# Kernel optimization log

Hardware: AMD Instinct MI355X
Metric: run time of the kernel (lower is better)

Reference implementation:

```python
import jax, jax.numpy as jnp
import numpy as np

B, N, QDIM, KVDIM, DIM, H = 2, 4096, 256, 256, 256, 8


def setup_inputs() -> dict:
    key = jax.random.key(0)
    ks = jax.random.split(key, 8)
    s = 0.02
    return {
        "x": jax.random.normal(ks[0], (B, N, QDIM), jnp.float32),
        "y": jax.random.normal(ks[1], (B, N, KVDIM), jnp.float32),
        "Wq": jax.random.normal(ks[2], (DIM, QDIM), jnp.float32) * s,
        "bq": jnp.zeros((DIM,), jnp.float32),
        "Wk": jax.random.normal(ks[3], (DIM, KVDIM), jnp.float32) * s,
        "bk": jnp.zeros((DIM,), jnp.float32),
        "Wv": jax.random.normal(ks[4], (DIM, KVDIM), jnp.float32) * s,
        "bv": jnp.zeros((DIM,), jnp.float32),
        "Wo": jax.random.normal(ks[5], (DIM, DIM), jnp.float32) * s,
        "bo": jnp.zeros((DIM,), jnp.float32),
    }


def reference(x, y, Wq, bq, Wk, bk, Wv, bv, Wo, bo):
    b, n, _ = x.shape
    h = H
    scale = KVDIM ** (-0.5)  # note: full kv_dim, as in the source
    q = x @ Wq.T + bq  # (b, n, dim)
    k = y @ Wk.T + bk
    v = y @ Wv.T + bv
    def split(t):
        return t.reshape(b, -1, h, DIM // h).transpose(0, 2, 1, 3)  # b h n d
    q, k, v = split(q), split(k), split(v)
    dots = jnp.einsum('bhid,bhjd->bhij', q, k) * scale
    attn = jax.nn.softmax(dots, axis=-1)
    out = jnp.einsum('bhij,bhjd->bhid', attn, v)
    out = out.transpose(0, 2, 1, 3).reshape(b, n, DIM)  # b n (h d)
    out = out @ Wo.T + bo
    return out
```

## Files before the change

kernel.cpp:

```cpp
#include <hip/hip_runtime.h>

#define BATCH 2
#define SEQ   4096
#define DIM   256
#define NHEAD 8
#define HDIM  32
#define ROWS  (BATCH * SEQ)

typedef __attribute__((ext_vector_type(8))) short short8;
typedef __attribute__((ext_vector_type(8))) unsigned short ushort8;
typedef __attribute__((ext_vector_type(4))) unsigned short ushortx4;
typedef __attribute__((ext_vector_type(4))) float floatx4;

static __device__ __forceinline__ unsigned short f2bf(float f) {
    union { float f; unsigned u; } v; v.f = f;
    unsigned r = v.u + 0x7fffu + ((v.u >> 16) & 1u);
    return (unsigned short)(r >> 16);
}

static __device__ __forceinline__ void g2l16(const void* g, void* l) {
    __builtin_amdgcn_global_load_lds(
        (const __attribute__((address_space(1))) unsigned int*)g,
        (__attribute__((address_space(3))) unsigned int*)l, 16, 0, 0);
}

__global__ __launch_bounds__(256) void convw_kernel(
    const float* __restrict__ W0, const float* __restrict__ W1,
    const float* __restrict__ W2, const float* __restrict__ W3,
    unsigned short* __restrict__ o0, unsigned short* __restrict__ o1,
    unsigned short* __restrict__ o2, unsigned short* __restrict__ o3) {
    const float* s; unsigned short* d;
    switch (blockIdx.y) {
        case 0:  s = W0; d = o0; break;
        case 1:  s = W1; d = o1; break;
        case 2:  s = W2; d = o2; break;
        default: s = W3; d = o3; break;
    }
    long off = ((long)blockIdx.x * 256 + threadIdx.x) * 4;
    float4 v = *(const float4*)(s + off);
    ushortx4 o;
    o.x = f2bf(v.x); o.y = f2bf(v.y); o.z = f2bf(v.z); o.w = f2bf(v.w);
    *(ushortx4*)(d + off) = o;
}

__global__ __launch_bounds__(256, 2) void qkv_kernel(
    const float* __restrict__ x, const float* __restrict__ y,
    const unsigned short* __restrict__ Wq, const unsigned short* __restrict__ Wk,
    const unsigned short* __restrict__ Wv,
    const float* __restrict__ bq, const float* __restrict__ bk, const float* __restrict__ bv,
    unsigned short* __restrict__ qo, unsigned short* __restrict__ ko,
    unsigned short* __restrict__ vto) {
    __shared__ unsigned short Abuf[8][64][32];
    const int tid = threadIdx.x, lane = tid & 63, wave = tid >> 6;
    const int ql = lane & 15, quad = lane >> 4;
    const int mat = blockIdx.y;
    const int m0 = blockIdx.x * 64;
    const float* A = (mat == 0) ? x : y;
    const unsigned short* W = (mat == 0) ? Wq : (mat == 1) ? Wk : Wv;
    const float* bias = (mat == 0) ? bq : (mat == 1) ? bk : bv;

    {
        const int row = tid >> 2, c8 = (tid & 3) * 8;
        const float* src = A + (long)(m0 + row) * DIM + c8;
#pragma unroll
        for (int kb = 0; kb < 8; kb++) {
            float4 v0 = *(const float4*)(src + kb * 32);
            float4 v1 = *(const float4*)(src + kb * 32 + 4);
            ushort8 o;
            o[0] = f2bf(v0.x); o[1] = f2bf(v0.y); o[2] = f2bf(v0.z); o[3] = f2bf(v0.w);
            o[4] = f2bf(v1.x); o[5] = f2bf(v1.y); o[6] = f2bf(v1.z); o[7] = f2bf(v1.w);
            *(ushort8*)(&Abuf[kb][row][c8]) = o;
        }
    }
    __syncthreads();
    const int n0 = wave * 64;
    floatx4 acc[4][4] = {};
    if (mat < 2) {
        for (int kb = 0; kb < 8; kb++) {
            short8 wf[4], af[4];
#pragma unroll
            for (int u = 0; u < 4; u++)
                wf[u] = *(const short8*)(W + (long)(n0 + u*16 + ql) * DIM + kb*32 + quad*8);
#pragma unroll
            for (int t = 0; t < 4; t++)
                af[t] = *(const short8*)(&Abuf[kb][t*16 + ql][quad*8]);
#pragma unroll
            for (int t = 0; t < 4; t++)
#pragma unroll
                for (int u = 0; u < 4; u++)
                    acc[t][u] = __builtin_amdgcn_mfma_f32_16x16x32_bf16(wf[u], af[t], acc[t][u], 0, 0, 0);
        }
        const float scale = (mat == 0) ? 0.09016844005556021f : 1.0f;
        unsigned short* out = (mat == 0) ? qo : ko;
#pragma unroll
        for (int t = 0; t < 4; t++) {
            int m = m0 + t*16 + ql;
#pragma unroll
            for (int u = 0; u < 4; u++) {
                int n = n0 + u*16 + quad*4;
                float4 b4 = *(const float4*)(bias + n);
                ushortx4 o;
                o.x = f2bf((acc[t][u][0] + b4.x) * scale);
                o.y = f2bf((acc[t][u][1] + b4.y) * scale);
                o.z = f2bf((acc[t][u][2] + b4.z) * scale);
                o.w = f2bf((acc[t][u][3] + b4.w) * scale);
                *(ushortx4*)(out + (long)m * DIM + n) = o;
            }
        }
    } else {
        for (int kb = 0; kb < 8; kb++) {
            short8 wf[4], af[4];
#pragma unroll
            for (int u = 0; u < 4; u++)
                wf[u] = *(const short8*)(W + (long)(n0 + u*16 + ql) * DIM + kb*32 + quad*8);
#pragma unroll
            for (int t = 0; t < 4; t++)
                af[t] = *(const short8*)(&Abuf[kb][t*16 + ql][quad*8]);
#pragma unroll
            for (int t = 0; t < 4; t++)
#pragma unroll
                for (int u = 0; u < 4; u++)
                    acc[t][u] = __builtin_amdgcn_mfma_f32_16x16x32_bf16(af[t], wf[u], acc[t][u], 0, 0, 0);
        }
#pragma unroll
        for (int t = 0; t < 4; t++) {
            int mb = m0 + t*16 + quad*4;
            int bi = mb >> 12, i0 = mb & (SEQ - 1);
#pragma unroll
            for (int u = 0; u < 4; u++) {
                int n = n0 + u*16 + ql;
                float b = bias[n];
                ushortx4 o;
                o.x = f2bf(acc[t][u][0] + b);
                o.y = f2bf(acc[t][u][1] + b);
                o.z = f2bf(acc[t][u][2] + b);
                o.w = f2bf(acc[t][u][3] + b);
                *(ushortx4*)(vto + ((long)(bi * DIM + n)) * SEQ + i0) = o;
            }
        }
    }
}

__global__ __launch_bounds__(256, 2) void attn_kernel(
    const unsigned short* __restrict__ qb, const unsigned short* __restrict__ kbuf,
    const unsigned short* __restrict__ vT, unsigned short* __restrict__ ao) {
    __shared__ unsigned short K0[128 * 32], K1[128 * 32];
    __shared__ unsigned short V0[32 * 128], V1[32 * 128];
    __shared__ unsigned short P[4][32][72];
    const int tid = threadIdx.x, lane = tid & 63, wave = tid >> 6;
    const int ql = lane & 15, quad = lane >> 4;
    const int bh = blockIdx.y, b = bh >> 3, h = bh & 7;
    const int q0 = blockIdx.x * 128 + wave * 32;

    const unsigned short* qrow = qb   + (long)b * SEQ * DIM + h * HDIM;
    const unsigned short* krow = kbuf + (long)b * SEQ * DIM + h * HDIM;
    const unsigned short* vrow = vT   + (long)(b * DIM + h * HDIM) * SEQ;

    short8 qf[2];
#pragma unroll
    for (int t = 0; t < 2; t++)
        qf[t] = *(const short8*)(qrow + (long)(q0 + t*16 + ql) * DIM + quad*8);

    const int kc0 = wave * 2, kc1 = wave * 2 + 1;
    const unsigned short* kg0 = krow + (long)(kc0*16 + (lane >> 2)) * DIM + (lane & 3) * 8;
    const unsigned short* kg1 = krow + (long)(kc1*16 + (lane >> 2)) * DIM + (lane & 3) * 8;
    const unsigned short* vg0 = vrow + (long)(kc0*4 + (lane >> 4)) * SEQ + (lane & 15) * 8;
    const unsigned short* vg1 = vrow + (long)(kc1*4 + (lane >> 4)) * SEQ + (lane & 15) * 8;

    floatx4 acc[2][2] = {};
    float lp[2] = {0.f, 0.f};

    auto stage = [&](unsigned short* Kd, unsigned short* Vd, int kv0) {
        g2l16(kg0 + (long)kv0 * DIM, Kd + kc0 * 512);
        g2l16(kg1 + (long)kv0 * DIM, Kd + kc1 * 512);
        g2l16(vg0 + kv0, Vd + kc0 * 512);
        g2l16(vg1 + kv0, Vd + kc1 * 512);
    };
    auto compute = [&](const unsigned short* Ks, const unsigned short* Vs) {
#pragma unroll
        for (int half = 0; half < 2; ++half) {
#pragma unroll
            for (int mt = 0; mt < 4; ++mt) {
                short8 kf = *(const short8*)(Ks + (half*64 + mt*16 + ql) * 32 + quad*8);
#pragma unroll
                for (int t = 0; t < 2; t++) {
                    floatx4 z = {};
                    floatx4 s = __builtin_amdgcn_mfma_f32_16x16x32_bf16(kf, qf[t], z, 0, 0, 0);
                    float p0 = __builtin_amdgcn_exp2f(s[0]);
                    float p1 = __builtin_amdgcn_exp2f(s[1]);
                    float p2 = __builtin_amdgcn_exp2f(s[2]);
                    float p3 = __builtin_amdgcn_exp2f(s[3]);
                    lp[t] += (p0 + p1) + (p2 + p3);
                    ushortx4 o;
                    o.x = f2bf(p0); o.y = f2bf(p1); o.z = f2bf(p2); o.w = f2bf(p3);
                    *(ushortx4*)(&P[wave][t*16 + ql][mt*16 + quad*4]) = o;
                }
            }
#pragma unroll
            for (int ks = 0; ks < 2; ++ks) {
                short8 pf[2];
#pragma unroll
                for (int t = 0; t < 2; t++)
                    pf[t] = *(const short8*)(&P[wave][t*16 + ql][ks*32 + quad*8]);
#pragma unroll
                for (int dt = 0; dt < 2; ++dt) {
                    short8 vf = *(const short8*)(Vs + (dt*16 + ql) * 128 + half*64 + ks*32 + quad*8);
#pragma unroll
                    for (int t = 0; t < 2; t++)
                        acc[dt][t] = __builtin_amdgcn_mfma_f32_16x16x32_bf16(vf, pf[t], acc[dt][t], 0, 0, 0);
                }
            }
        }
    };

    stage(K0, V0, 0);
    __syncthreads();
    for (int it = 0; it < SEQ / 128; it += 2) {
        if (it + 1 < SEQ / 128) stage(K1, V1, (it + 1) * 128);
        compute(K0, V0);
        __syncthreads();
        if (it + 2 < SEQ / 128) stage(K0, V0, (it + 2) * 128);
        compute(K1, V1);
        __syncthreads();
    }

    float inv[2];
#pragma unroll
    for (int t = 0; t < 2; t++) {
        float l = lp[t];
        l += __shfl_xor(l, 16, 64);
        l += __shfl_xor(l, 32, 64);
        inv[t] = 1.0f / l;
    }
#pragma unroll
    for (int dt = 0; dt < 2; dt++)
#pragma unroll
        for (int t = 0; t < 2; t++) {
            ushortx4 o;
            o.x = f2bf(acc[dt][t][0] * inv[t]);
            o.y = f2bf(acc[dt][t][1] * inv[t]);
            o.z = f2bf(acc[dt][t][2] * inv[t]);
            o.w = f2bf(acc[dt][t][3] * inv[t]);
            *(ushortx4*)(ao + (long)(b*SEQ + q0 + t*16 + ql) * DIM + h*HDIM + dt*16 + quad*4) = o;
        }
}

__global__ __launch_bounds__(256, 2) void oproj_kernel(
    const unsigned short* __restrict__ A, const unsigned short* __restrict__ W,
    const float* __restrict__ bias, float* __restrict__ out) {
    __shared__ unsigned short Abuf[8][64][32];
    const int tid = threadIdx.x, lane = tid & 63, wave = tid >> 6;
    const int ql = lane & 15, quad = lane >> 4;
    const int m0 = blockIdx.x * 64;
#pragma unroll
    for (int j = 0; j < 8; j++) {
        int c = wave * 8 + j;
        int kb = c >> 2, r0 = (c & 3) * 16;
        const unsigned short* g = A + (long)(m0 + r0 + (lane >> 2)) * DIM + kb*32 + (lane & 3) * 8;
        g2l16(g, &Abuf[kb][r0][0]);
    }
    __syncthreads();
    const int n0 = wave * 64;
    floatx4 acc[4][4] = {};
    for (int kb = 0; kb < 8; kb++) {
        short8 wf[4], af[4];
#pragma unroll
        for (int u = 0; u < 4; u++)
            wf[u] = *(const short8*)(W + (long)(n0 + u*16 + ql) * DIM + kb*32 + quad*8);
#pragma unroll
        for (int t = 0; t < 4; t++)
            af[t] = *(const short8*)(&Abuf[kb][t*16 + ql][quad*8]);
#pragma unroll
        for (int t = 0; t < 4; t++)
#pragma unroll
            for (int u = 0; u < 4; u++)
                acc[t][u] = __builtin_amdgcn_mfma_f32_16x16x32_bf16(wf[u], af[t], acc[t][u], 0, 0, 0);
    }
#pragma unroll
    for (int t = 0; t < 4; t++) {
        int m = m0 + t*16 + ql;
#pragma unroll
        for (int u = 0; u < 4; u++) {
            int n = n0 + u*16 + quad*4;
            float4 b4 = *(const float4*)(bias + n);
            float4 o;
            o.x = acc[t][u][0] + b4.x;
            o.y = acc[t][u][1] + b4.y;
            o.z = acc[t][u][2] + b4.z;
            o.w = acc[t][u][3] + b4.w;
            *(float4*)(out + (long)m * DIM + n) = o;
        }
    }
}

extern "C" void kernel_launch(void* const* d_in, const int* in_sizes, int n_in,
                              void* d_out, int out_size, void* d_ws, size_t ws_size,
                              hipStream_t stream) {
    const float* x  = (const float*)d_in[0];
    const float* y  = (const float*)d_in[1];
    const float* Wq = (const float*)d_in[2];
    const float* bq = (const float*)d_in[3];
    const float* Wk = (const float*)d_in[4];
    const float* bk = (const float*)d_in[5];
    const float* Wv = (const float*)d_in[6];
    const float* bv = (const float*)d_in[7];
    const float* Wo = (const float*)d_in[8];
    const float* bo = (const float*)d_in[9];
    float* out = (float*)d_out;

    const long NX = (long)ROWS * DIM;
    const long NW = (long)DIM * DIM;
    unsigned short* Wqb  = (unsigned short*)d_ws;
    unsigned short* Wkb  = Wqb + NW;
    unsigned short* Wvb  = Wkb + NW;
    unsigned short* Wob  = Wvb + NW;
    unsigned short* qbf  = Wob + NW;
    unsigned short* kbf  = qbf + NX;
    unsigned short* vTb  = kbf + NX;
    unsigned short* attn = vTb + NX;

    convw_kernel<<<dim3(NW / 1024, 4), dim3(256), 0, stream>>>(
        Wq, Wk, Wv, Wo, Wqb, Wkb, Wvb, Wob);

    qkv_kernel<<<dim3(ROWS / 64, 3), dim3(256), 0, stream>>>(
        x, y, Wqb, Wkb, Wvb, bq, bk, bv, qbf, kbf, vTb);

    attn_kernel<<<dim3(SEQ / 128, BATCH * NHEAD), dim3(256), 0, stream>>>(
        qbf, kbf, vTb, attn);

    oproj_kernel<<<dim3(ROWS / 64), dim3(256), 0, stream>>>(
        attn, Wob, bo, out);
}
```

Before: 189.8 us.

## Fuse weight conversion into GEMMs, swizzle LDS, compute softmax row sums via MFMA

```diff
diff --git a/kernel.cpp b/kernel.cpp
--- a/kernel.cpp
+++ b/kernel.cpp
@@ -11,12 +11,19 @@
 typedef __attribute__((ext_vector_type(8))) unsigned short ushort8;
 typedef __attribute__((ext_vector_type(4))) unsigned short ushortx4;
 typedef __attribute__((ext_vector_type(4))) float floatx4;
+typedef __attribute__((ext_vector_type(2))) unsigned int uintx2;
 
 static __device__ __forceinline__ unsigned short f2bf(float f) {
     union { float f; unsigned u; } v; v.f = f;
     unsigned r = v.u + 0x7fffu + ((v.u >> 16) & 1u);
     return (unsigned short)(r >> 16);
 }
+static __device__ __forceinline__ unsigned fbits(float f) {
+    union { float f; unsigned u; } v; v.f = f; return v.u;
+}
+static __device__ __forceinline__ unsigned pack2(float a, float b) {
+    return __builtin_amdgcn_perm(fbits(b), fbits(a), 0x07060302u);
+}
 
 static __device__ __forceinline__ void g2l16(const void* g, void* l) {
     __builtin_amdgcn_global_load_lds(
@@ -24,29 +31,10 @@
         (__attribute__((address_space(3))) unsigned int*)l, 16, 0, 0);
 }
 
-__global__ __launch_bounds__(256) void convw_kernel(
-    const float* __restrict__ W0, const float* __restrict__ W1,
-    const float* __restrict__ W2, const float* __restrict__ W3,
-    unsigned short* __restrict__ o0, unsigned short* __restrict__ o1,
-    unsigned short* __restrict__ o2, unsigned short* __restrict__ o3) {
-    const float* s; unsigned short* d;
-    switch (blockIdx.y) {
-        case 0:  s = W0; d = o0; break;
-        case 1:  s = W1; d = o1; break;
-        case 2:  s = W2; d = o2; break;
-        default: s = W3; d = o3; break;
-    }
-    long off = ((long)blockIdx.x * 256 + threadIdx.x) * 4;
-    float4 v = *(const float4*)(s + off);
-    ushortx4 o;
-    o.x = f2bf(v.x); o.y = f2bf(v.y); o.z = f2bf(v.z); o.w = f2bf(v.w);
-    *(ushortx4*)(d + off) = o;
-}
-
 __global__ __launch_bounds__(256, 2) void qkv_kernel(
     const float* __restrict__ x, const float* __restrict__ y,
-    const unsigned short* __restrict__ Wq, const unsigned short* __restrict__ Wk,
-    const unsigned short* __restrict__ Wv,
+    const float* __restrict__ Wq, const float* __restrict__ Wk,
+    const float* __restrict__ Wv,
     const float* __restrict__ bq, const float* __restrict__ bk, const float* __restrict__ bv,
     unsigned short* __restrict__ qo, unsigned short* __restrict__ ko,
     unsigned short* __restrict__ vto) {
@@ -56,11 +44,12 @@
     const int mat = blockIdx.y;
     const int m0 = blockIdx.x * 64;
     const float* A = (mat == 0) ? x : y;
-    const unsigned short* W = (mat == 0) ? Wq : (mat == 1) ? Wk : Wv;
+    const float* W = (mat == 0) ? Wq : (mat == 1) ? Wk : Wv;
     const float* bias = (mat == 0) ? bq : (mat == 1) ? bk : bv;
 
     {
         const int row = tid >> 2, c8 = (tid & 3) * 8;
+        const int swz = ((tid & 3) ^ ((row >> 1) & 3)) * 8;
         const float* src = A + (long)(m0 + row) * DIM + c8;
 #pragma unroll
         for (int kb = 0; kb < 8; kb++) {
@@ -69,27 +58,43 @@
             ushort8 o;
             o[0] = f2bf(v0.x); o[1] = f2bf(v0.y); o[2] = f2bf(v0.z); o[3] = f2bf(v0.w);
             o[4] = f2bf(v1.x); o[5] = f2bf(v1.y); o[6] = f2bf(v1.z); o[7] = f2bf(v1.w);
-            *(ushort8*)(&Abuf[kb][row][c8]) = o;
+            *(ushort8*)(&Abuf[kb][row][swz]) = o;
         }
     }
     __syncthreads();
     const int n0 = wave * 64;
+    const int akey = (quad ^ ((ql >> 1) & 3)) * 8;
     floatx4 acc[4][4] = {};
-    if (mat < 2) {
-        for (int kb = 0; kb < 8; kb++) {
-            short8 wf[4], af[4];
-#pragma unroll
-            for (int u = 0; u < 4; u++)
-                wf[u] = *(const short8*)(W + (long)(n0 + u*16 + ql) * DIM + kb*32 + quad*8);
-#pragma unroll
-            for (int t = 0; t < 4; t++)
-                af[t] = *(const short8*)(&Abuf[kb][t*16 + ql][quad*8]);
+    for (int kb = 0; kb < 8; kb++) {
+        short8 wf[4], af[4];
+#pragma unroll
+        for (int u = 0; u < 4; u++) {
+            const float* wr = W + (long)(n0 + u*16 + ql) * DIM + kb*32 + quad*8;
+            float4 a = *(const float4*)wr;
+            float4 c = *(const float4*)(wr + 4);
+            short8 o;
+            o[0] = (short)f2bf(a.x); o[1] = (short)f2bf(a.y); o[2] = (short)f2bf(a.z); o[3] = (short)f2bf(a.w);
+            o[4] = (short)f2bf(c.x); o[5] = (short)f2bf(c.y); o[6] = (short)f2bf(c.z); o[7] = (short)f2bf(c.w);
+            wf[u] = o;
+        }
+#pragma unroll
+        for (int t = 0; t < 4; t++)
+            af[t] = *(const short8*)(&Abuf[kb][t*16 + ql][akey]);
+        if (mat < 2) {
 #pragma unroll
             for (int t = 0; t < 4; t++)
 #pragma unroll
                 for (int u = 0; u < 4; u++)
                     acc[t][u] = __builtin_amdgcn_mfma_f32_16x16x32_bf16(wf[u], af[t], acc[t][u], 0, 0, 0);
-        }
+        } else {
+#pragma unroll
+            for (int t = 0; t < 4; t++)
+#pragma unroll
+                for (int u = 0; u < 4; u++)
+                    acc[t][u] = __builtin_amdgcn_mfma_f32_16x16x32_bf16(af[t], wf[u], acc[t][u], 0, 0, 0);
+        }
+    }
+    if (mat < 2) {
         const float scale = (mat == 0) ? 0.09016844005556021f : 1.0f;
         unsigned short* out = (mat == 0) ? qo : ko;
 #pragma unroll
@@ -108,20 +113,6 @@
             }
         }
     } else {
-        for (int kb = 0; kb < 8; kb++) {
-            short8 wf[4], af[4];
-#pragma unroll
-            for (int u = 0; u < 4; u++)
-                wf[u] = *(const short8*)(W + (long)(n0 + u*16 + ql) * DIM + kb*32 + quad*8);
-#pragma unroll
-            for (int t = 0; t < 4; t++)
-                af[t] = *(const short8*)(&Abuf[kb][t*16 + ql][quad*8]);
-#pragma unroll
-            for (int t = 0; t < 4; t++)
-#pragma unroll
-                for (int u = 0; u < 4; u++)
-                    acc[t][u] = __builtin_amdgcn_mfma_f32_16x16x32_bf16(af[t], wf[u], acc[t][u], 0, 0, 0);
-        }
 #pragma unroll
         for (int t = 0; t < 4; t++) {
             int mb = m0 + t*16 + quad*4;
@@ -161,14 +152,25 @@
     for (int t = 0; t < 2; t++)
         qf[t] = *(const short8*)(qrow + (long)(q0 + t*16 + ql) * DIM + quad*8);
 
+    short8 ones;
+#pragma unroll
+    for (int i = 0; i < 8; i++) ones[i] = (short)0x3F80;
+
     const int kc0 = wave * 2, kc1 = wave * 2 + 1;
-    const unsigned short* kg0 = krow + (long)(kc0*16 + (lane >> 2)) * DIM + (lane & 3) * 8;
-    const unsigned short* kg1 = krow + (long)(kc1*16 + (lane >> 2)) * DIM + (lane & 3) * 8;
-    const unsigned short* vg0 = vrow + (long)(kc0*4 + (lane >> 4)) * SEQ + (lane & 15) * 8;
-    const unsigned short* vg1 = vrow + (long)(kc1*4 + (lane >> 4)) * SEQ + (lane & 15) * 8;
+    const int klr = lane >> 2, kswz = ((lane & 3) ^ ((lane >> 3) & 3)) * 8;
+    const unsigned short* kg0 = krow + (long)(kc0*16 + klr) * DIM + kswz;
+    const unsigned short* kg1 = krow + (long)(kc1*16 + klr) * DIM + kswz;
+    const int vlr = lane >> 4, vcl = lane & 15;
+    const int vsw0 = (vcl ^ ((kc0*4 + vlr) & 7)) * 8;
+    const int vsw1 = (vcl ^ ((kc1*4 + vlr) & 7)) * 8;
+    const unsigned short* vg0 = vrow + (long)(kc0*4 + vlr) * SEQ + vsw0;
+    const unsigned short* vg1 = vrow + (long)(kc1*4 + vlr) * SEQ + vsw1;
+
+    const int kro = (quad ^ ((ql >> 1) & 3)) * 8;
+    const int vmask = ql & 7;
 
     floatx4 acc[2][2] = {};
-    float lp[2] = {0.f, 0.f};
+    floatx4 accL[2] = {};
 
     auto stage = [&](unsigned short* Kd, unsigned short* Vd, int kv0) {
         g2l16(kg0 + (long)kv0 * DIM, Kd + kc0 * 512);
@@ -181,7 +183,7 @@
         for (int half = 0; half < 2; ++half) {
 #pragma unroll
             for (int mt = 0; mt < 4; ++mt) {
-                short8 kf = *(const short8*)(Ks + (half*64 + mt*16 + ql) * 32 + quad*8);
+                short8 kf = *(const short8*)(Ks + (half*64 + mt*16 + ql) * 32 + kro);
 #pragma unroll
                 for (int t = 0; t < 2; t++) {
                     floatx4 z = {};
@@ -190,10 +192,10 @@
                     float p1 = __builtin_amdgcn_exp2f(s[1]);
                     float p2 = __builtin_amdgcn_exp2f(s[2]);
                     float p3 = __builtin_amdgcn_exp2f(s[3]);
-                    lp[t] += (p0 + p1) + (p2 + p3);
-                    ushortx4 o;
-                    o.x = f2bf(p0); o.y = f2bf(p1); o.z = f2bf(p2); o.w = f2bf(p3);
-                    *(ushortx4*)(&P[wave][t*16 + ql][mt*16 + quad*4]) = o;
+                    uintx2 w;
+                    w.x = pack2(p0, p1);
+                    w.y = pack2(p2, p3);
+                    *(uintx2*)(&P[wave][t*16 + ql][mt*16 + quad*4]) = w;
                 }
             }
 #pragma unroll
@@ -203,8 +205,12 @@
                 for (int t = 0; t < 2; t++)
                     pf[t] = *(const short8*)(&P[wave][t*16 + ql][ks*32 + quad*8]);
 #pragma unroll
+                for (int t = 0; t < 2; t++)
+                    accL[t] = __builtin_amdgcn_mfma_f32_16x16x32_bf16(ones, pf[t], accL[t], 0, 0, 0);
+#pragma unroll
                 for (int dt = 0; dt < 2; ++dt) {
-                    short8 vf = *(const short8*)(Vs + (dt*16 + ql) * 128 + half*64 + ks*32 + quad*8);
+                    int vco = ((8*half + 4*ks + quad) ^ vmask) * 8;
+                    short8 vf = *(const short8*)(Vs + (dt*16 + ql) * 128 + vco);
 #pragma unroll
                     for (int t = 0; t < 2; t++)
                         acc[dt][t] = __builtin_amdgcn_mfma_f32_16x16x32_bf16(vf, pf[t], acc[dt][t], 0, 0, 0);
@@ -226,12 +232,7 @@
 
     float inv[2];
 #pragma unroll
-    for (int t = 0; t < 2; t++) {
-        float l = lp[t];
-        l += __shfl_xor(l, 16, 64);
-        l += __shfl_xor(l, 32, 64);
-        inv[t] = 1.0f / l;
-    }
+    for (int t = 0; t < 2; t++) inv[t] = 1.0f / accL[t][0];
 #pragma unroll
     for (int dt = 0; dt < 2; dt++)
 #pragma unroll
@@ -246,38 +247,47 @@
 }
 
 __global__ __launch_bounds__(256, 2) void oproj_kernel(
-    const unsigned short* __restrict__ A, const unsigned short* __restrict__ W,
+    const unsigned short* __restrict__ A, const float* __restrict__ W,
     const float* __restrict__ bias, float* __restrict__ out) {
-    __shared__ unsigned short Abuf[8][64][32];
+    __shared__ unsigned short Abuf[8][32][32];
     const int tid = threadIdx.x, lane = tid & 63, wave = tid >> 6;
     const int ql = lane & 15, quad = lane >> 4;
-    const int m0 = blockIdx.x * 64;
-#pragma unroll
-    for (int j = 0; j < 8; j++) {
-        int c = wave * 8 + j;
-        int kb = c >> 2, r0 = (c & 3) * 16;
-        const unsigned short* g = A + (long)(m0 + r0 + (lane >> 2)) * DIM + kb*32 + (lane & 3) * 8;
-        g2l16(g, &Abuf[kb][r0][0]);
+    const int m0 = blockIdx.x * 32;
+    const int swz = ((lane & 3) ^ ((lane >> 3) & 3)) * 8;
+#pragma unroll
+    for (int j = 0; j < 4; j++) {
+        int c = wave * 4 + j;
+        int kb = c >> 1, hf = (c & 1) * 16;
+        const unsigned short* g = A + (long)(m0 + hf + (lane >> 2)) * DIM + kb*32 + swz;
+        g2l16(g, &Abuf[kb][hf][0]);
     }
     __syncthreads();
     const int n0 = wave * 64;
-    floatx4 acc[4][4] = {};
+    const int akey = (quad ^ ((ql >> 1) & 3)) * 8;
+    floatx4 acc[2][4] = {};
     for (int kb = 0; kb < 8; kb++) {
-        short8 wf[4], af[4];
-#pragma unroll
-        for (int u = 0; u < 4; u++)
-            wf[u] = *(const short8*)(W + (long)(n0 + u*16 + ql) * DIM + kb*32 + quad*8);
-#pragma unroll
-        for (int t = 0; t < 4; t++)
-            af[t] = *(const short8*)(&Abuf[kb][t*16 + ql][quad*8]);
-#pragma unroll
-        for (int t = 0; t < 4; t++)
+        short8 wf[4], af[2];
+#pragma unroll
+        for (int u = 0; u < 4; u++) {
+            const float* wr = W + (long)(n0 + u*16 + ql) * DIM + kb*32 + quad*8;
+            float4 a = *(const float4*)wr;
+            float4 c = *(const float4*)(wr + 4);
+            short8 o;
+            o[0] = (short)f2bf(a.x); o[1] = (short)f2bf(a.y); o[2] = (short)f2bf(a.z); o[3] = (short)f2bf(a.w);
+            o[4] = (short)f2bf(c.x); o[5] = (short)f2bf(c.y); o[6] = (short)f2bf(c.z); o[7] = (short)f2bf(c.w);
+            wf[u] = o;
+        }
+#pragma unroll
+        for (int t = 0; t < 2; t++)
+            af[t] = *(const short8*)(&Abuf[kb][t*16 + ql][akey]);
+#pragma unroll
+        for (int t = 0; t < 2; t++)
 #pragma unroll
             for (int u = 0; u < 4; u++)
                 acc[t][u] = __builtin_amdgcn_mfma_f32_16x16x32_bf16(wf[u], af[t], acc[t][u], 0, 0, 0);
     }
 #pragma unroll
-    for (int t = 0; t < 4; t++) {
+    for (int t = 0; t < 2; t++) {
         int m = m0 + t*16 + ql;
 #pragma unroll
         for (int u = 0; u < 4; u++) {
@@ -309,25 +319,17 @@
     float* out = (float*)d_out;
 
     const long NX = (long)ROWS * DIM;
-    const long NW = (long)DIM * DIM;
-    unsigned short* Wqb  = (unsigned short*)d_ws;
-    unsigned short* Wkb  = Wqb + NW;
-    unsigned short* Wvb  = Wkb + NW;
-    unsigned short* Wob  = Wvb + NW;
-    unsigned short* qbf  = Wob + NW;
+    unsigned short* qbf  = (unsigned short*)d_ws;
     unsigned short* kbf  = qbf + NX;
     unsigned short* vTb  = kbf + NX;
     unsigned short* attn = vTb + NX;
 
-    convw_kernel<<<dim3(NW / 1024, 4), dim3(256), 0, stream>>>(
-        Wq, Wk, Wv, Wo, Wqb, Wkb, Wvb, Wob);
-
     qkv_kernel<<<dim3(ROWS / 64, 3), dim3(256), 0, stream>>>(
-        x, y, Wqb, Wkb, Wvb, bq, bk, bv, qbf, kbf, vTb);
+        x, y, Wq, Wk, Wv, bq, bk, bv, qbf, kbf, vTb);
 
     attn_kernel<<<dim3(SEQ / 128, BATCH * NHEAD), dim3(256), 0, stream>>>(
         qbf, kbf, vTb, attn);
 
-    oproj_kernel<<<dim3(ROWS / 64), dim3(256), 0, stream>>>(
-        attn, Wob, bo, out);
-}
+    oproj_kernel<<<dim3(ROWS / 32), dim3(256), 0, stream>>>(
+        attn, Wo, bo, out);
+}
```

Result: faster. 169.9 us (-10.5%).

## Swizzle LDS layouts, shrink attention KV tile, compute row sums via MFMA

Applied to the files above, without the earlier changes.

```diff
diff --git a/kernel.cpp b/kernel.cpp
--- a/kernel.cpp
+++ b/kernel.cpp
@@ -11,13 +11,19 @@
 typedef __attribute__((ext_vector_type(8))) unsigned short ushort8;
 typedef __attribute__((ext_vector_type(4))) unsigned short ushortx4;
 typedef __attribute__((ext_vector_type(4))) float floatx4;
+typedef __attribute__((ext_vector_type(2))) unsigned int uintx2;
 
 static __device__ __forceinline__ unsigned short f2bf(float f) {
     union { float f; unsigned u; } v; v.f = f;
     unsigned r = v.u + 0x7fffu + ((v.u >> 16) & 1u);
     return (unsigned short)(r >> 16);
 }
-
+static __device__ __forceinline__ unsigned fbits(float f) {
+    union { float f; unsigned u; } v; v.f = f; return v.u;
+}
+static __device__ __forceinline__ unsigned pack2(float a, float b) {
+    return __builtin_amdgcn_perm(fbits(b), fbits(a), 0x07060302u);
+}
 static __device__ __forceinline__ void g2l16(const void* g, void* l) {
     __builtin_amdgcn_global_load_lds(
         (const __attribute__((address_space(1))) unsigned int*)g,
@@ -61,6 +67,7 @@
 
     {
         const int row = tid >> 2, c8 = (tid & 3) * 8;
+        const int swz = ((tid & 3) ^ ((row >> 1) & 3)) * 8;
         const float* src = A + (long)(m0 + row) * DIM + c8;
 #pragma unroll
         for (int kb = 0; kb < 8; kb++) {
@@ -69,27 +76,36 @@
             ushort8 o;
             o[0] = f2bf(v0.x); o[1] = f2bf(v0.y); o[2] = f2bf(v0.z); o[3] = f2bf(v0.w);
             o[4] = f2bf(v1.x); o[5] = f2bf(v1.y); o[6] = f2bf(v1.z); o[7] = f2bf(v1.w);
-            *(ushort8*)(&Abuf[kb][row][c8]) = o;
+            *(ushort8*)(&Abuf[kb][row][swz]) = o;
         }
     }
     __syncthreads();
     const int n0 = wave * 64;
+    const int akey = (quad ^ ((ql >> 1) & 3)) * 8;
     floatx4 acc[4][4] = {};
-    if (mat < 2) {
-        for (int kb = 0; kb < 8; kb++) {
-            short8 wf[4], af[4];
-#pragma unroll
-            for (int u = 0; u < 4; u++)
-                wf[u] = *(const short8*)(W + (long)(n0 + u*16 + ql) * DIM + kb*32 + quad*8);
-#pragma unroll
-            for (int t = 0; t < 4; t++)
-                af[t] = *(const short8*)(&Abuf[kb][t*16 + ql][quad*8]);
+    for (int kb = 0; kb < 8; kb++) {
+        short8 wf[4], af[4];
+#pragma unroll
+        for (int u = 0; u < 4; u++)
+            wf[u] = *(const short8*)(W + (long)(n0 + u*16 + ql) * DIM + kb*32 + quad*8);
+#pragma unroll
+        for (int t = 0; t < 4; t++)
+            af[t] = *(const short8*)(&Abuf[kb][t*16 + ql][akey]);
+        if (mat < 2) {
 #pragma unroll
             for (int t = 0; t < 4; t++)
 #pragma unroll
                 for (int u = 0; u < 4; u++)
                     acc[t][u] = __builtin_amdgcn_mfma_f32_16x16x32_bf16(wf[u], af[t], acc[t][u], 0, 0, 0);
-        }
+        } else {
+#pragma unroll
+            for (int t = 0; t < 4; t++)
+#pragma unroll
+                for (int u = 0; u < 4; u++)
+                    acc[t][u] = __builtin_amdgcn_mfma_f32_16x16x32_bf16(af[t], wf[u], acc[t][u], 0, 0, 0);
+        }
+    }
+    if (mat < 2) {
         const float scale = (mat == 0) ? 0.09016844005556021f : 1.0f;
         unsigned short* out = (mat == 0) ? qo : ko;
 #pragma unroll
@@ -108,20 +124,6 @@
             }
         }
     } else {
-        for (int kb = 0; kb < 8; kb++) {
-            short8 wf[4], af[4];
-#pragma unroll
-            for (int u = 0; u < 4; u++)
-                wf[u] = *(const short8*)(W + (long)(n0 + u*16 + ql) * DIM + kb*32 + quad*8);
-#pragma unroll
-            for (int t = 0; t < 4; t++)
-                af[t] = *(const short8*)(&Abuf[kb][t*16 + ql][quad*8]);
-#pragma unroll
-            for (int t = 0; t < 4; t++)
-#pragma unroll
-                for (int u = 0; u < 4; u++)
-                    acc[t][u] = __builtin_amdgcn_mfma_f32_16x16x32_bf16(af[t], wf[u], acc[t][u], 0, 0, 0);
-        }
 #pragma unroll
         for (int t = 0; t < 4; t++) {
             int mb = m0 + t*16 + quad*4;
@@ -141,11 +143,11 @@
     }
 }
 
-__global__ __launch_bounds__(256, 2) void attn_kernel(
+__global__ __launch_bounds__(256, 4) void attn_kernel(
     const unsigned short* __restrict__ qb, const unsigned short* __restrict__ kbuf,
     const unsigned short* __restrict__ vT, unsigned short* __restrict__ ao) {
-    __shared__ unsigned short K0[128 * 32], K1[128 * 32];
-    __shared__ unsigned short V0[32 * 128], V1[32 * 128];
+    __shared__ unsigned short K0[64 * 32], K1[64 * 32];
+    __shared__ unsigned short V0[32 * 64], V1[32 * 64];
     __shared__ unsigned short P[4][32][72];
     const int tid = threadIdx.x, lane = tid & 63, wave = tid >> 6;
     const int ql = lane & 15, quad = lane >> 4;
@@ -161,77 +163,79 @@
     for (int t = 0; t < 2; t++)
         qf[t] = *(const short8*)(qrow + (long)(q0 + t*16 + ql) * DIM + quad*8);
 
-    const int kc0 = wave * 2, kc1 = wave * 2 + 1;
-    const unsigned short* kg0 = krow + (long)(kc0*16 + (lane >> 2)) * DIM + (lane & 3) * 8;
-    const unsigned short* kg1 = krow + (long)(kc1*16 + (lane >> 2)) * DIM + (lane & 3) * 8;
-    const unsigned short* vg0 = vrow + (long)(kc0*4 + (lane >> 4)) * SEQ + (lane & 15) * 8;
-    const unsigned short* vg1 = vrow + (long)(kc1*4 + (lane >> 4)) * SEQ + (lane & 15) * 8;
+    short8 ones;
+#pragma unroll
+    for (int i = 0; i < 8; i++) ones[i] = (short)0x3F80;
+
+    const unsigned short* kg = krow + (long)(wave*16 + (lane >> 2)) * DIM
+                                    + ((lane & 3) ^ ((lane >> 3) & 3)) * 8;
+    const unsigned short* vg = vrow + (long)(wave*8 + (lane >> 3)) * SEQ
+                                    + ((lane & 7) ^ (lane >> 3)) * 8;
+    unsigned short* kd0 = K0 + wave * 512;  unsigned short* kd1 = K1 + wave * 512;
+    unsigned short* vd0 = V0 + wave * 512;  unsigned short* vd1 = V1 + wave * 512;
+    const int kro = (quad ^ ((ql >> 1) & 3)) * 8;
+    const int vmask = ql & 7;
 
     floatx4 acc[2][2] = {};
-    float lp[2] = {0.f, 0.f};
-
-    auto stage = [&](unsigned short* Kd, unsigned short* Vd, int kv0) {
-        g2l16(kg0 + (long)kv0 * DIM, Kd + kc0 * 512);
-        g2l16(kg1 + (long)kv0 * DIM, Kd + kc1 * 512);
-        g2l16(vg0 + kv0, Vd + kc0 * 512);
-        g2l16(vg1 + kv0, Vd + kc1 * 512);
+    floatx4 accL[2] = {};
+
+    auto compute = [&](const unsigned short* Ks, const unsigned short* Vs) {
+#pragma unroll
+        for (int mt = 0; mt < 4; ++mt) {
+            short8 kf = *(const short8*)(Ks + (mt*16 + ql) * 32 + kro);
+#pragma unroll
+            for (int t = 0; t < 2; t++) {
+                floatx4 z = {};
+                floatx4 s = __builtin_amdgcn_mfma_f32_16x16x32_bf16(kf, qf[t], z, 0, 0, 0);
+                float p0 = __builtin_amdgcn_exp2f(s[0]);
+                float p1 = __builtin_amdgcn_exp2f(s[1]);
+                float p2 = __builtin_amdgcn_exp2f(s[2]);
+                float p3 = __builtin_amdgcn_exp2f(s[3]);
+                uintx2 w;
+                w.x = pack2(p0, p1);
+                w.y = pack2(p2, p3);
+                *(uintx2*)(&P[wave][t*16 + ql][mt*16 + quad*4]) = w;
+            }
+        }
+#pragma unroll
+        for (int ks = 0; ks < 2; ++ks) {
+            short8 pf[2];
+#pragma unroll
+            for (int t = 0; t < 2; t++)
+                pf[t] = *(const short8*)(&P[wave][t*16 + ql][ks*32 + quad*8]);
+#pragma unroll
+            for (int t = 0; t < 2; t++)
+                accL[t] = __builtin_amdgcn_mfma_f32_16x16x32_bf16(ones, pf[t], accL[t], 0, 0, 0);
+#pragma unroll
+            for (int dt = 0; dt < 2; ++dt) {
+                short8 vf = *(const short8*)(Vs + (dt*16 + ql) * 64 + ((ks*4 + quad) ^ vmask) * 8);
+#pragma unroll
+                for (int t = 0; t < 2; t++)
+                    acc[dt][t] = __builtin_amdgcn_mfma_f32_16x16x32_bf16(vf, pf[t], acc[dt][t], 0, 0, 0);
+            }
+        }
     };
-    auto compute = [&](const unsigned short* Ks, const unsigned short* Vs) {
-#pragma unroll
-        for (int half = 0; half < 2; ++half) {
-#pragma unroll
-            for (int mt = 0; mt < 4; ++mt) {
-                short8 kf = *(const short8*)(Ks + (half*64 + mt*16 + ql) * 32 + quad*8);
-#pragma unroll
-                for (int t = 0; t < 2; t++) {
-                    floatx4 z = {};
-                    floatx4 s = __builtin_amdgcn_mfma_f32_16x16x32_bf16(kf, qf[t], z, 0, 0, 0);
-                    float p0 = __builtin_amdgcn_exp2f(s[0]);
-                    float p1 = __builtin_amdgcn_exp2f(s[1]);
-                    float p2 = __builtin_amdgcn_exp2f(s[2]);
-                    float p3 = __builtin_amdgcn_exp2f(s[3]);
-                    lp[t] += (p0 + p1) + (p2 + p3);
-                    ushortx4 o;
-                    o.x = f2bf(p0); o.y = f2bf(p1); o.z = f2bf(p2); o.w = f2bf(p3);
-                    *(ushortx4*)(&P[wave][t*16 + ql][mt*16 + quad*4]) = o;
-                }
-            }
-#pragma unroll
-            for (int ks = 0; ks < 2; ++ks) {
-                short8 pf[2];
-#pragma unroll
-                for (int t = 0; t < 2; t++)
-                    pf[t] = *(const short8*)(&P[wave][t*16 + ql][ks*32 + quad*8]);
-#pragma unroll
-                for (int dt = 0; dt < 2; ++dt) {
-                    short8 vf = *(const short8*)(Vs + (dt*16 + ql) * 128 + half*64 + ks*32 + quad*8);
-#pragma unroll
-                    for (int t = 0; t < 2; t++)
-                        acc[dt][t] = __builtin_amdgcn_mfma_f32_16x16x32_bf16(vf, pf[t], acc[dt][t], 0, 0, 0);
-                }
-            }
-        }
-    };
-
-    stage(K0, V0, 0);
+
+    g2l16(kg, kd0); g2l16(vg, vd0);
     __syncthreads();
-    for (int it = 0; it < SEQ / 128; it += 2) {
-        if (it + 1 < SEQ / 128) stage(K1, V1, (it + 1) * 128);
+    for (int it = 0; it < SEQ / 64; it += 2) {
+        if (it + 1 < SEQ / 64) {
+            g2l16(kg + (long)(it + 1) * 64 * DIM, kd1);
+            g2l16(vg + (it + 1) * 64, vd1);
+        }
         compute(K0, V0);
         __syncthreads();
-        if (it + 2 < SEQ / 128) stage(K0, V0, (it + 2) * 128);
+        if (it + 2 < SEQ / 64) {
+            g2l16(kg + (long)(it + 2) * 64 * DIM, kd0);
+            g2l16(vg + (it + 2) * 64, vd0);
+        }
         compute(K1, V1);
         __syncthreads();
     }
 
     float inv[2];
 #pragma unroll
-    for (int t = 0; t < 2; t++) {
-        float l = lp[t];
-        l += __shfl_xor(l, 16, 64);
-        l += __shfl_xor(l, 32, 64);
-        inv[t] = 1.0f / l;
-    }
+    for (int t = 0; t < 2; t++) inv[t] = 1.0f / accL[t][0];
 #pragma unroll
     for (int dt = 0; dt < 2; dt++)
 #pragma unroll
@@ -252,15 +256,17 @@
     const int tid = threadIdx.x, lane = tid & 63, wave = tid >> 6;
     const int ql = lane & 15, quad = lane >> 4;
     const int m0 = blockIdx.x * 64;
+    const int swz = ((lane & 3) ^ ((lane >> 3) & 3)) * 8;
 #pragma unroll
     for (int j = 0; j < 8; j++) {
         int c = wave * 8 + j;
         int kb = c >> 2, r0 = (c & 3) * 16;
-        const unsigned short* g = A + (long)(m0 + r0 + (lane >> 2)) * DIM + kb*32 + (lane & 3) * 8;
+        const unsigned short* g = A + (long)(m0 + r0 + (lane >> 2)) * DIM + kb*32 + swz;
         g2l16(g, &Abuf[kb][r0][0]);
     }
     __syncthreads();
     const int n0 = wave * 64;
+    const int akey = (quad ^ ((ql >> 1) & 3)) * 8;
     floatx4 acc[4][4] = {};
     for (int kb = 0; kb < 8; kb++) {
         short8 wf[4], af[4];
@@ -269,7 +275,7 @@
             wf[u] = *(const short8*)(W + (long)(n0 + u*16 + ql) * DIM + kb*32 + quad*8);
 #pragma unroll
         for (int t = 0; t < 4; t++)
-            af[t] = *(const short8*)(&Abuf[kb][t*16 + ql][quad*8]);
+            af[t] = *(const short8*)(&Abuf[kb][t*16 + ql][akey]);
 #pragma unroll
         for (int t = 0; t < 4; t++)
 #pragma unroll
```

New measurement: 164.4 us. 13.4% less time.
